# Kernel optimization log

Measured on AMD Instinct MI355X. Metric: run time of the kernel, lower is better.

Reference implementation:

```python
import jax, jax.numpy as jnp
import numpy as np

EPS = 1e-5

def layer_norm(x, g, b):
    m = jnp.mean(x, axis=-1, keepdims=True)
    v = jnp.var(x, axis=-1, keepdims=True)
    return (x - m) * jax.lax.rsqrt(v + EPS) * g + b

def setup_inputs() -> dict:
    key = jax.random.key(0)
    ks = jax.random.split(key, 16)
    B, N, C_Z, C_H = 1, 512, 128, 128
    s_z = 1.0 / np.sqrt(C_Z)
    s_h = 1.0 / np.sqrt(C_H)
    inp = {
        "z": jax.random.normal(ks[0], (B, N, N, C_Z), jnp.float32),
        "mask": jnp.ones((B, N, N), jnp.float32),
        # linear weights stored as [in, out] so forward is x @ W + b
        "w_ag": jax.random.uniform(ks[1], (C_Z, C_H), jnp.float32, -s_z, s_z),
        "b_ag": jnp.zeros((C_H,), jnp.float32),
        "w_ap": jax.random.uniform(ks[2], (C_Z, C_H), jnp.float32, -s_z, s_z),
        "b_ap": jnp.zeros((C_H,), jnp.float32),
        "w_bg": jax.random.uniform(ks[3], (C_Z, C_H), jnp.float32, -s_z, s_z),
        "b_bg": jnp.zeros((C_H,), jnp.float32),
        "w_bp": jax.random.uniform(ks[4], (C_Z, C_H), jnp.float32, -s_z, s_z),
        "b_bp": jnp.zeros((C_H,), jnp.float32),
        "w_g": jax.random.uniform(ks[5], (C_Z, C_Z), jnp.float32, -s_z, s_z),
        "b_g": jnp.zeros((C_Z,), jnp.float32),
        "w_z": jax.random.uniform(ks[6], (C_H, C_Z), jnp.float32, -s_h, s_h),
        "b_z": jnp.zeros((C_Z,), jnp.float32),
        "ln_in_g": jnp.ones((C_Z,), jnp.float32),
        "ln_in_b": jnp.zeros((C_Z,), jnp.float32),
        "ln_out_g": jnp.ones((C_H,), jnp.float32),
        "ln_out_b": jnp.zeros((C_H,), jnp.float32),
    }
    return inp

def reference(z, mask, w_ag, b_ag, w_ap, b_ap, w_bg, b_bg, w_bp, b_bp,
              w_g, b_g, w_z, b_z, ln_in_g, ln_in_b, ln_out_g, ln_out_b):
    m = mask[..., None]                      # [B,N,N,1]
    zn = layer_norm(z, ln_in_g, ln_in_b)     # [B,N,N,Cz]
    a = m * jax.nn.sigmoid(zn @ w_ag + b_ag) * (zn @ w_ap + b_ap)  # [B,N,N,Ch]
    b = m * jax.nn.sigmoid(zn @ w_bg + b_bg) * (zn @ w_bp + b_bp)  # [B,N,N,Ch]
    # outgoing: p[i,j,c] = sum_k a[i,k,c] * b[j,k,c]
    x = jnp.einsum('bikc,bjkc->bijc', a, b)
    x = layer_norm(x, ln_out_g, ln_out_b)
    x = x @ w_z + b_z
    g = jax.nn.sigmoid(zn @ w_g + b_g)
    return x * g
```

## Files before the change

kernel.cpp:

```cpp
#include <hip/hip_runtime.h>
#include <hip/hip_bf16.h>
#include <math.h>


#define N 512
#define C 128
#define NN (N*N)
#define PK 136
#define PT 40
#define PX 137

typedef __attribute__((ext_vector_type(8))) short bf16x8;
typedef __attribute__((ext_vector_type(4))) float f32x4;
typedef unsigned short u16;
typedef unsigned int u32;

__device__ __forceinline__ u16 f2bf(float f) {
    u32 u = __builtin_bit_cast(u32, f);
    u = (u + 0x7fffu + ((u >> 16) & 1u)) >> 16;
    return (u16)u;
}
__device__ __forceinline__ float bf2f(u16 h) {
    return __builtin_bit_cast(float, ((u32)h) << 16);
}
__device__ __forceinline__ float sigmoidf(float x) {
    return 1.f / (1.f + __expf(-x));
}

__global__ __launch_bounds__(256) void k_wt_all(
    const float* __restrict__ w0, const float* __restrict__ w1,
    const float* __restrict__ w2, const float* __restrict__ w3,
    const float* __restrict__ w4, const float* __restrict__ w5,
    u16* __restrict__ o0, u16* __restrict__ o1, u16* __restrict__ o2,
    u16* __restrict__ o3, u16* __restrict__ o4, u16* __restrict__ o5) {
    int sel = blockIdx.x >> 6;
    int idx = (blockIdx.x & 63) * 256 + threadIdx.x;
    const float* w = sel == 0 ? w0 : sel == 1 ? w1 : sel == 2 ? w2
                   : sel == 3 ? w3 : sel == 4 ? w4 : w5;
    u16* o = sel == 0 ? o0 : sel == 1 ? o1 : sel == 2 ? o2
           : sel == 3 ? o3 : sel == 4 ? o4 : o5;
    int co = idx >> 7, k = idx & 127;
    o[idx] = f2bf(w[k * C + co]);
}

__global__ __launch_bounds__(256) void k_proj_fused(
    const float* __restrict__ z, const float* __restrict__ mask,
    const float* __restrict__ lg, const float* __restrict__ lb,
    const u16* __restrict__ wag, const float* __restrict__ bag,
    const u16* __restrict__ wap, const float* __restrict__ bap,
    const u16* __restrict__ wbg, const float* __restrict__ bbg,
    const u16* __restrict__ wbp, const float* __restrict__ bbp,
    const u16* __restrict__ wgg, const float* __restrict__ bgg,
    u16* __restrict__ aT, u16* __restrict__ bT, u16* __restrict__ gate) {
    __shared__ u16 sA[64 * PK];
    __shared__ u16 sT[128 * 72];
    long r0 = (long)blockIdx.x * 64;
    int tid = threadIdx.x, wave = tid >> 6, lane = tid & 63;
    int lo = lane & 15, quad = lane >> 4;

    {
        int c = lane * 2;
        float g0 = lg[c], g1 = lg[c + 1], b0 = lb[c], b1 = lb[c + 1];
        for (int rr = 0; rr < 16; ++rr) {
            int row = wave * 16 + rr;
            float2 xv = *(const float2*)(z + (r0 + row) * C + c);
            float s = xv.x + xv.y, s2 = xv.x * xv.x + xv.y * xv.y;
#pragma unroll
            for (int off = 32; off; off >>= 1) {
                s += __shfl_xor(s, off);
                s2 += __shfl_xor(s2, off);
            }
            float mean = s * (1.f / 128.f);
            float var = s2 * (1.f / 128.f) - mean * mean;
            float rs = rsqrtf(var + 1e-5f);
            float y0 = (xv.x - mean) * rs * g0 + b0;
            float y1 = (xv.y - mean) * rs * g1 + b1;
            *(u32*)(&sA[row * PK + c]) = (u32)f2bf(y0) | ((u32)f2bf(y1) << 16);
        }
    }
    __syncthreads();

    int c0 = wave * 32;
    float msk[4][4];
#pragma unroll
    for (int mi = 0; mi < 4; ++mi)
#pragma unroll
        for (int r = 0; r < 4; ++r)
            msk[mi][r] = mask[r0 + mi * 16 + quad * 4 + r];

    auto pair_stage = [&](const u16* __restrict__ wG, const float* __restrict__ bG,
                          const u16* __restrict__ wP, const float* __restrict__ bP,
                          u16* __restrict__ outT) {
        bf16x8 fG[2][4], fP[2][4];
#pragma unroll
        for (int nt = 0; nt < 2; ++nt)
#pragma unroll
            for (int ki = 0; ki < 4; ++ki) {
                fG[nt][ki] = *(const bf16x8*)(wG + (c0 + nt * 16 + lo) * C + ki * 32 + quad * 8);
                fP[nt][ki] = *(const bf16x8*)(wP + (c0 + nt * 16 + lo) * C + ki * 32 + quad * 8);
            }
        f32x4 aG[4][2], aP[4][2];
#pragma unroll
        for (int mi = 0; mi < 4; ++mi)
#pragma unroll
            for (int nt = 0; nt < 2; ++nt) { aG[mi][nt] = (f32x4)(0.f); aP[mi][nt] = (f32x4)(0.f); }
#pragma unroll
        for (int mi = 0; mi < 4; ++mi)
#pragma unroll
            for (int ki = 0; ki < 4; ++ki) {
                bf16x8 av = *(const bf16x8*)(&sA[(mi * 16 + lo) * PK + ki * 32 + quad * 8]);
#pragma unroll
                for (int nt = 0; nt < 2; ++nt) {
                    aG[mi][nt] = __builtin_amdgcn_mfma_f32_16x16x32_bf16(av, fG[nt][ki], aG[mi][nt], 0, 0, 0);
                    aP[mi][nt] = __builtin_amdgcn_mfma_f32_16x16x32_bf16(av, fP[nt][ki], aP[mi][nt], 0, 0, 0);
                }
            }
#pragma unroll
        for (int nt = 0; nt < 2; ++nt) {
            int c = c0 + nt * 16 + lo;
            float bGv = bG[c], bPv = bP[c];
#pragma unroll
            for (int mi = 0; mi < 4; ++mi)
#pragma unroll
                for (int r = 0; r < 4; ++r) {
                    int row = mi * 16 + quad * 4 + r;
                    float val = msk[mi][r] * sigmoidf(aG[mi][nt][r] + bGv) * (aP[mi][nt][r] + bPv);
                    sT[c * 72 + row] = f2bf(val);
                }
        }
        __syncthreads();
#pragma unroll
        for (int p = 0; p < 4; ++p) {
            int linear = p * 2048 + tid * 8;
            int cc = linear >> 6, row = linear & 63;
            *(uint4*)(outT + (long)cc * NN + r0 + row) = *(const uint4*)(&sT[cc * 72 + row]);
        }
        __syncthreads();
    };
    pair_stage(wag, bag, wap, bap, aT);
    pair_stage(wbg, bbg, wbp, bbp, bT);

    {
        bf16x8 fG[2][4];
#pragma unroll
        for (int nt = 0; nt < 2; ++nt)
#pragma unroll
            for (int ki = 0; ki < 4; ++ki)
                fG[nt][ki] = *(const bf16x8*)(wgg + (c0 + nt * 16 + lo) * C + ki * 32 + quad * 8);
        f32x4 aG[4][2];
#pragma unroll
        for (int mi = 0; mi < 4; ++mi)
#pragma unroll
            for (int nt = 0; nt < 2; ++nt) aG[mi][nt] = (f32x4)(0.f);
#pragma unroll
        for (int mi = 0; mi < 4; ++mi)
#pragma unroll
            for (int ki = 0; ki < 4; ++ki) {
                bf16x8 av = *(const bf16x8*)(&sA[(mi * 16 + lo) * PK + ki * 32 + quad * 8]);
#pragma unroll
                for (int nt = 0; nt < 2; ++nt)
                    aG[mi][nt] = __builtin_amdgcn_mfma_f32_16x16x32_bf16(av, fG[nt][ki], aG[mi][nt], 0, 0, 0);
            }
        __syncthreads();
#pragma unroll
        for (int nt = 0; nt < 2; ++nt) {
            int c = c0 + nt * 16 + lo;
            float bv = bgg[c];
#pragma unroll
            for (int mi = 0; mi < 4; ++mi)
#pragma unroll
                for (int r = 0; r < 4; ++r) {
                    int row = mi * 16 + quad * 4 + r;
                    sA[row * PK + c] = f2bf(sigmoidf(aG[mi][nt][r] + bv));
                }
        }
        __syncthreads();
#pragma unroll
        for (int p = 0; p < 4; ++p) {
            int linear = p * 2048 + tid * 8;
            int row = linear >> 7, k = linear & 127;
            *(uint4*)(gate + (r0 + row) * C + k) = *(const uint4*)(&sA[row * PK + k]);
        }
    }
}

__global__ __launch_bounds__(256) void k_tri(const u16* __restrict__ aT,
                                             const u16* __restrict__ bT,
                                             u16* __restrict__ xT) {
    __shared__ u16 sA[128 * PT];
    __shared__ u16 sB[128 * PT];
    int c = blockIdx.y;
    int i0 = (blockIdx.x >> 2) * 128, j0 = (blockIdx.x & 3) * 128;
    const u16* aBase = aT + (long)c * NN + (long)i0 * N;
    const u16* bBase = bT + (long)c * NN + (long)j0 * N;
    int tid = threadIdx.x;
    int wave = tid >> 6, lane = tid & 63, lo = lane & 15, quad = lane >> 4;
    int mq = (wave >> 1) * 64, nq = (wave & 1) * 64;
    f32x4 acc[4][4];
#pragma unroll
    for (int mi = 0; mi < 4; ++mi)
#pragma unroll
        for (int ni = 0; ni < 4; ++ni) acc[mi][ni] = (f32x4)(0.f);
    for (int kk = 0; kk < N; kk += 32) {
        __syncthreads();
#pragma unroll
        for (int p = 0; p < 2; ++p) {
            int linear = p * 2048 + tid * 8;
            int row = linear >> 5, k = linear & 31;
            *(uint4*)(&sA[row * PT + k]) = *(const uint4*)(aBase + row * N + kk + k);
            *(uint4*)(&sB[row * PT + k]) = *(const uint4*)(bBase + row * N + kk + k);
        }
        __syncthreads();
        bf16x8 af[4], bfr[4];
#pragma unroll
        for (int mi = 0; mi < 4; ++mi)
            af[mi] = *(const bf16x8*)(&sA[(mq + mi * 16 + lo) * PT + quad * 8]);
#pragma unroll
        for (int ni = 0; ni < 4; ++ni)
            bfr[ni] = *(const bf16x8*)(&sB[(nq + ni * 16 + lo) * PT + quad * 8]);
#pragma unroll
        for (int mi = 0; mi < 4; ++mi)
#pragma unroll
            for (int ni = 0; ni < 4; ++ni)
                acc[mi][ni] = __builtin_amdgcn_mfma_f32_16x16x32_bf16(af[mi], bfr[ni], acc[mi][ni], 0, 0, 0);
    }
    u16* outBase = xT + (long)c * NN;
#pragma unroll
    for (int mi = 0; mi < 4; ++mi)
#pragma unroll
        for (int ni = 0; ni < 4; ++ni)
#pragma unroll
            for (int r = 0; r < 4; ++r) {
                int gi = i0 + mq + mi * 16 + quad * 4 + r;
                int gj = j0 + nq + ni * 16 + lo;
                outBase[(long)gi * N + gj] = f2bf(acc[mi][ni][r]);
            }
}

__global__ __launch_bounds__(256) void k_out(
    const u16* __restrict__ xT, const u16* __restrict__ gate,
    const u16* __restrict__ wzT, const float* __restrict__ bz,
    const float* __restrict__ lg, const float* __restrict__ lb,
    float* __restrict__ out) {
    __shared__ float sX[64 * PX];
    __shared__ u16 sA[64 * PK];
    __shared__ float sRed[2][4][64];
    __shared__ float2 sMV[64];
    long r0 = (long)blockIdx.x * 64;
    int tid = threadIdx.x;
#pragma unroll
    for (int p = 0; p < 4; ++p) {
        int linear = p * 2048 + tid * 8;
        int cc = linear >> 6, jr = linear & 63;
        uint4 v = *(const uint4*)(xT + (long)cc * NN + r0 + jr);
        u16* u = (u16*)&v;
#pragma unroll
        for (int e = 0; e < 8; ++e) sX[(jr + e) * PX + cc] = bf2f(u[e]);
    }
    __syncthreads();
    {
        int jr = tid & 63, part = tid >> 6;
        float s = 0, s2 = 0;
#pragma unroll
        for (int c = part * 32; c < part * 32 + 32; ++c) {
            float v = sX[jr * PX + c];
            s += v; s2 += v * v;
        }
        sRed[0][part][jr] = s; sRed[1][part][jr] = s2;
    }
    __syncthreads();
    if (tid < 64) {
        float S = 0, S2 = 0;
#pragma unroll
        for (int p = 0; p < 4; ++p) { S += sRed[0][p][tid]; S2 += sRed[1][p][tid]; }
        float mean = S * (1.f / 128.f);
        float var = S2 * (1.f / 128.f) - mean * mean;
        sMV[tid] = make_float2(mean, rsqrtf(var + 1e-5f));
    }
    __syncthreads();
    {
        int row = tid & 63, c0 = (tid >> 6) * 32;
        float2 mv = sMV[row];
#pragma unroll
        for (int c = c0; c < c0 + 32; ++c) {
            float v = (sX[row * PX + c] - mv.x) * mv.y * lg[c] + lb[c];
            sA[row * PK + c] = f2bf(v);
        }
    }
    __syncthreads();
    int wave = tid >> 6, lane = tid & 63, lo = lane & 15, quad = lane >> 4;
    int msub = wave * 16;
    bf16x8 av[4];
#pragma unroll
    for (int ki = 0; ki < 4; ++ki)
        av[ki] = *(const bf16x8*)(&sA[(msub + lo) * PK + ki * 32 + quad * 8]);
    f32x4 acc[8];
#pragma unroll
    for (int nt = 0; nt < 8; ++nt) acc[nt] = (f32x4)(0.f);
#pragma unroll
    for (int nt = 0; nt < 8; ++nt)
#pragma unroll
        for (int ki = 0; ki < 4; ++ki) {
            bf16x8 b8 = *(const bf16x8*)(wzT + (nt * 16 + lo) * C + ki * 32 + quad * 8);
            acc[nt] = __builtin_amdgcn_mfma_f32_16x16x32_bf16(av[ki], b8, acc[nt], 0, 0, 0);
        }
#pragma unroll
    for (int nt = 0; nt < 8; ++nt) {
        int c = nt * 16 + lo;
        float bzv = bz[c];
#pragma unroll
        for (int r = 0; r < 4; ++r) {
            int row = msub + quad * 4 + r;
            long rr = r0 + row;
            float g = bf2f(gate[rr * C + c]);
            out[rr * C + c] = (acc[nt][r] + bzv) * g;
        }
    }
}

extern "C" void kernel_launch(void* const* d_in, const int* in_sizes, int n_in,
                              void* d_out, int out_size, void* d_ws, size_t ws_size,
                              hipStream_t stream) {
    const float* z       = (const float*)d_in[0];
    const float* mask    = (const float*)d_in[1];
    const float* w_ag    = (const float*)d_in[2];
    const float* b_ag    = (const float*)d_in[3];
    const float* w_ap    = (const float*)d_in[4];
    const float* b_ap    = (const float*)d_in[5];
    const float* w_bg    = (const float*)d_in[6];
    const float* b_bg    = (const float*)d_in[7];
    const float* w_bp    = (const float*)d_in[8];
    const float* b_bp    = (const float*)d_in[9];
    const float* w_g     = (const float*)d_in[10];
    const float* b_g     = (const float*)d_in[11];
    const float* w_z     = (const float*)d_in[12];
    const float* b_z     = (const float*)d_in[13];
    const float* ln_in_g = (const float*)d_in[14];
    const float* ln_in_b = (const float*)d_in[15];
    const float* ln_out_g= (const float*)d_in[16];
    const float* ln_out_b= (const float*)d_in[17];
    float* out = (float*)d_out;

    char* ws = (char*)d_ws;
    u16* a_t  = (u16*)(ws);
    u16* b_t  = (u16*)(ws + 67108864L);
    u16* gate = (u16*)(ws + 134217728L);
    u16* x_t  = (u16*)(ws + 201326592L);
    u16* wag_t = (u16*)(ws + 268435456L);
    u16* wap_t = wag_t + 16384;
    u16* wbg_t = wag_t + 32768;
    u16* wbp_t = wag_t + 49152;
    u16* wg_t  = wag_t + 65536;
    u16* wz_t  = wag_t + 81920;

    k_wt_all<<<384, 256, 0, stream>>>(w_ag, w_ap, w_bg, w_bp, w_g, w_z,
                                      wag_t, wap_t, wbg_t, wbp_t, wg_t, wz_t);

    k_proj_fused<<<NN / 64, 256, 0, stream>>>(
        z, mask, ln_in_g, ln_in_b,
        wag_t, b_ag, wap_t, b_ap, wbg_t, b_bg, wbp_t, b_bp, wg_t, b_g,
        a_t, b_t, gate);

    k_tri<<<dim3(16, 128), 256, 0, stream>>>(a_t, b_t, x_t);

    k_out<<<NN / 64, 256, 0, stream>>>(x_t, gate, wz_t, b_z, ln_out_g, ln_out_b, out);
}
```

Measured before the change: 585.6 us.

## Fold layernorm affine into weights, per-wave transposes, prefetch and swizzle tri kernel

The layernorm gamma/beta are folded into the bf16 projection weights and into precomputed biases (a new k_bias kernel), so the projection and output kernels only normalize. The input layernorm now uses float4 loads with four lanes per row, and the projection kernel transposes through a small per-wave shared buffer instead of block-wide barriers. The triangle kernel gains register prefetch of the next k-tile and a swizzled 1D grid for better cache locality. These changes remove per-element affine work, reduce barriers, and hide global latency, at the cost of an extra small kernel launch and extra register pressure.

```diff
diff --git a/kernel.cpp b/kernel.cpp
--- a/kernel.cpp
+++ b/kernel.cpp
@@ -9,6 +9,7 @@
 #define PK 136
 #define PT 40
 #define PX 137
+#define ST 72
 
 typedef __attribute__((ext_vector_type(8))) short bf16x8;
 typedef __attribute__((ext_vector_type(4))) float f32x4;
@@ -31,6 +32,7 @@
     const float* __restrict__ w0, const float* __restrict__ w1,
     const float* __restrict__ w2, const float* __restrict__ w3,
     const float* __restrict__ w4, const float* __restrict__ w5,
+    const float* __restrict__ gin, const float* __restrict__ gout,
     u16* __restrict__ o0, u16* __restrict__ o1, u16* __restrict__ o2,
     u16* __restrict__ o3, u16* __restrict__ o4, u16* __restrict__ o5) {
     int sel = blockIdx.x >> 6;
@@ -39,43 +41,70 @@
                    : sel == 3 ? w3 : sel == 4 ? w4 : w5;
     u16* o = sel == 0 ? o0 : sel == 1 ? o1 : sel == 2 ? o2
            : sel == 3 ? o3 : sel == 4 ? o4 : o5;
+    const float* g = (sel == 5) ? gout : gin;
     int co = idx >> 7, k = idx & 127;
-    o[idx] = f2bf(w[k * C + co]);
+    o[idx] = f2bf(g[k] * w[k * C + co]);
+}
+
+__global__ __launch_bounds__(256) void k_bias(
+    const float* __restrict__ w0, const float* __restrict__ w1,
+    const float* __restrict__ w2, const float* __restrict__ w3,
+    const float* __restrict__ w4, const float* __restrict__ w5,
+    const float* __restrict__ b0, const float* __restrict__ b1,
+    const float* __restrict__ b2, const float* __restrict__ b3,
+    const float* __restrict__ b4, const float* __restrict__ b5,
+    const float* __restrict__ vin, const float* __restrict__ vout,
+    float* __restrict__ obias) {
+    int id = blockIdx.x * 256 + threadIdx.x;
+    int m = id >> 7, cc = id & 127;
+    const float* w = m == 0 ? w0 : m == 1 ? w1 : m == 2 ? w2
+                   : m == 3 ? w3 : m == 4 ? w4 : w5;
+    const float* b = m == 0 ? b0 : m == 1 ? b1 : m == 2 ? b2
+                   : m == 3 ? b3 : m == 4 ? b4 : b5;
+    const float* v = (m == 5) ? vout : vin;
+    float acc = 0.f;
+#pragma unroll 4
+    for (int k = 0; k < 128; ++k) acc += v[k] * w[k * C + cc];
+    obias[id] = b[cc] + acc;
 }
 
 __global__ __launch_bounds__(256) void k_proj_fused(
     const float* __restrict__ z, const float* __restrict__ mask,
-    const float* __restrict__ lg, const float* __restrict__ lb,
-    const u16* __restrict__ wag, const float* __restrict__ bag,
-    const u16* __restrict__ wap, const float* __restrict__ bap,
-    const u16* __restrict__ wbg, const float* __restrict__ bbg,
-    const u16* __restrict__ wbp, const float* __restrict__ bbp,
-    const u16* __restrict__ wgg, const float* __restrict__ bgg,
+    const u16* __restrict__ wag, const u16* __restrict__ wap,
+    const u16* __restrict__ wbg, const u16* __restrict__ wbp,
+    const u16* __restrict__ wgg, const float* __restrict__ biasAll,
     u16* __restrict__ aT, u16* __restrict__ bT, u16* __restrict__ gate) {
     __shared__ u16 sA[64 * PK];
-    __shared__ u16 sT[128 * 72];
+    __shared__ u16 sT[4][16 * ST];
     long r0 = (long)blockIdx.x * 64;
     int tid = threadIdx.x, wave = tid >> 6, lane = tid & 63;
     int lo = lane & 15, quad = lane >> 4;
 
     {
-        int c = lane * 2;
-        float g0 = lg[c], g1 = lg[c + 1], b0 = lb[c], b1 = lb[c + 1];
-        for (int rr = 0; rr < 16; ++rr) {
-            int row = wave * 16 + rr;
-            float2 xv = *(const float2*)(z + (r0 + row) * C + c);
-            float s = xv.x + xv.y, s2 = xv.x * xv.x + xv.y * xv.y;
-#pragma unroll
-            for (int off = 32; off; off >>= 1) {
-                s += __shfl_xor(s, off);
-                s2 += __shfl_xor(s2, off);
-            }
-            float mean = s * (1.f / 128.f);
-            float var = s2 * (1.f / 128.f) - mean * mean;
-            float rs = rsqrtf(var + 1e-5f);
-            float y0 = (xv.x - mean) * rs * g0 + b0;
-            float y1 = (xv.y - mean) * rs * g1 + b1;
-            *(u32*)(&sA[row * PK + c]) = (u32)f2bf(y0) | ((u32)f2bf(y1) << 16);
+        int rl = lane >> 2, cb = lane & 3;
+        int row = wave * 16 + rl;
+        const float* zr = z + (r0 + row) * C + cb * 32;
+        float4 v[8];
+        float s = 0.f, s2 = 0.f;
+#pragma unroll
+        for (int i = 0; i < 8; ++i) {
+            v[i] = *(const float4*)(zr + i * 4);
+            s  += v[i].x + v[i].y + v[i].z + v[i].w;
+            s2 += v[i].x * v[i].x + v[i].y * v[i].y + v[i].z * v[i].z + v[i].w * v[i].w;
+        }
+        s += __shfl_xor(s, 1); s2 += __shfl_xor(s2, 1);
+        s += __shfl_xor(s, 2); s2 += __shfl_xor(s2, 2);
+        float mean = s * (1.f / 128.f);
+        float rs = rsqrtf(s2 * (1.f / 128.f) - mean * mean + 1e-5f);
+        u16* dst = &sA[row * PK + cb * 32];
+#pragma unroll
+        for (int j = 0; j < 4; ++j) {
+            uint4 pk;
+            pk.x = (u32)f2bf((v[2*j].x   - mean) * rs) | ((u32)f2bf((v[2*j].y   - mean) * rs) << 16);
+            pk.y = (u32)f2bf((v[2*j].z   - mean) * rs) | ((u32)f2bf((v[2*j].w   - mean) * rs) << 16);
+            pk.z = (u32)f2bf((v[2*j+1].x - mean) * rs) | ((u32)f2bf((v[2*j+1].y - mean) * rs) << 16);
+            pk.w = (u32)f2bf((v[2*j+1].z - mean) * rs) | ((u32)f2bf((v[2*j+1].w - mean) * rs) << 16);
+            *(uint4*)(dst + 8 * j) = pk;
         }
     }
     __syncthreads();
@@ -87,92 +116,86 @@
 #pragma unroll
         for (int r = 0; r < 4; ++r)
             msk[mi][r] = mask[r0 + mi * 16 + quad * 4 + r];
+
+    u16* sTw = &sT[wave][0];
 
     auto pair_stage = [&](const u16* __restrict__ wG, const float* __restrict__ bG,
                           const u16* __restrict__ wP, const float* __restrict__ bP,
                           u16* __restrict__ outT) {
-        bf16x8 fG[2][4], fP[2][4];
-#pragma unroll
-        for (int nt = 0; nt < 2; ++nt)
-#pragma unroll
-            for (int ki = 0; ki < 4; ++ki) {
-                fG[nt][ki] = *(const bf16x8*)(wG + (c0 + nt * 16 + lo) * C + ki * 32 + quad * 8);
-                fP[nt][ki] = *(const bf16x8*)(wP + (c0 + nt * 16 + lo) * C + ki * 32 + quad * 8);
-            }
-        f32x4 aG[4][2], aP[4][2];
-#pragma unroll
-        for (int mi = 0; mi < 4; ++mi)
-#pragma unroll
-            for (int nt = 0; nt < 2; ++nt) { aG[mi][nt] = (f32x4)(0.f); aP[mi][nt] = (f32x4)(0.f); }
-#pragma unroll
-        for (int mi = 0; mi < 4; ++mi)
-#pragma unroll
-            for (int ki = 0; ki < 4; ++ki) {
-                bf16x8 av = *(const bf16x8*)(&sA[(mi * 16 + lo) * PK + ki * 32 + quad * 8]);
-#pragma unroll
-                for (int nt = 0; nt < 2; ++nt) {
-                    aG[mi][nt] = __builtin_amdgcn_mfma_f32_16x16x32_bf16(av, fG[nt][ki], aG[mi][nt], 0, 0, 0);
-                    aP[mi][nt] = __builtin_amdgcn_mfma_f32_16x16x32_bf16(av, fP[nt][ki], aP[mi][nt], 0, 0, 0);
-                }
-            }
 #pragma unroll
         for (int nt = 0; nt < 2; ++nt) {
             int c = c0 + nt * 16 + lo;
+            bf16x8 fG[4], fP[4];
+#pragma unroll
+            for (int ki = 0; ki < 4; ++ki) {
+                fG[ki] = *(const bf16x8*)(wG + c * C + ki * 32 + quad * 8);
+                fP[ki] = *(const bf16x8*)(wP + c * C + ki * 32 + quad * 8);
+            }
+            f32x4 aG[4], aP[4];
+#pragma unroll
+            for (int mi = 0; mi < 4; ++mi) { aG[mi] = (f32x4)(0.f); aP[mi] = (f32x4)(0.f); }
+#pragma unroll
+            for (int mi = 0; mi < 4; ++mi)
+#pragma unroll
+                for (int ki = 0; ki < 4; ++ki) {
+                    bf16x8 av = *(const bf16x8*)(&sA[(mi * 16 + lo) * PK + ki * 32 + quad * 8]);
+                    aG[mi] = __builtin_amdgcn_mfma_f32_16x16x32_bf16(av, fG[ki], aG[mi], 0, 0, 0);
+                    aP[mi] = __builtin_amdgcn_mfma_f32_16x16x32_bf16(av, fP[ki], aP[mi], 0, 0, 0);
+                }
             float bGv = bG[c], bPv = bP[c];
 #pragma unroll
+            for (int mi = 0; mi < 4; ++mi) {
+                float v0 = msk[mi][0] * sigmoidf(aG[mi][0] + bGv) * (aP[mi][0] + bPv);
+                float v1 = msk[mi][1] * sigmoidf(aG[mi][1] + bGv) * (aP[mi][1] + bPv);
+                float v2 = msk[mi][2] * sigmoidf(aG[mi][2] + bGv) * (aP[mi][2] + bPv);
+                float v3 = msk[mi][3] * sigmoidf(aG[mi][3] + bGv) * (aP[mi][3] + bPv);
+                uint2 pk;
+                pk.x = (u32)f2bf(v0) | ((u32)f2bf(v1) << 16);
+                pk.y = (u32)f2bf(v2) | ((u32)f2bf(v3) << 16);
+                *(uint2*)(&sTw[lo * ST + mi * 16 + quad * 4]) = pk;
+            }
+            {
+                int cl = lane >> 2, pr = lane & 3;
+                uint4 x0 = *(const uint4*)(&sTw[cl * ST + pr * 16]);
+                uint4 x1 = *(const uint4*)(&sTw[cl * ST + pr * 16 + 8]);
+                u16* g = outT + (long)(c0 + nt * 16 + cl) * NN + r0 + pr * 16;
+                *(uint4*)(g) = x0;
+                *(uint4*)(g + 8) = x1;
+            }
+        }
+    };
+    pair_stage(wag, biasAll + 0,   wap, biasAll + 128, aT);
+    pair_stage(wbg, biasAll + 256, wbp, biasAll + 384, bT);
+
+    {
+        f32x4 gA[2][4];
+#pragma unroll
+        for (int nt = 0; nt < 2; ++nt) {
+            bf16x8 gF[4];
+#pragma unroll
+            for (int ki = 0; ki < 4; ++ki)
+                gF[ki] = *(const bf16x8*)(wgg + (c0 + nt * 16 + lo) * C + ki * 32 + quad * 8);
+#pragma unroll
+            for (int mi = 0; mi < 4; ++mi) gA[nt][mi] = (f32x4)(0.f);
+#pragma unroll
             for (int mi = 0; mi < 4; ++mi)
 #pragma unroll
-                for (int r = 0; r < 4; ++r) {
-                    int row = mi * 16 + quad * 4 + r;
-                    float val = msk[mi][r] * sigmoidf(aG[mi][nt][r] + bGv) * (aP[mi][nt][r] + bPv);
-                    sT[c * 72 + row] = f2bf(val);
+                for (int ki = 0; ki < 4; ++ki) {
+                    bf16x8 av = *(const bf16x8*)(&sA[(mi * 16 + lo) * PK + ki * 32 + quad * 8]);
+                    gA[nt][mi] = __builtin_amdgcn_mfma_f32_16x16x32_bf16(av, gF[ki], gA[nt][mi], 0, 0, 0);
                 }
         }
         __syncthreads();
-#pragma unroll
-        for (int p = 0; p < 4; ++p) {
-            int linear = p * 2048 + tid * 8;
-            int cc = linear >> 6, row = linear & 63;
-            *(uint4*)(outT + (long)cc * NN + r0 + row) = *(const uint4*)(&sT[cc * 72 + row]);
-        }
-        __syncthreads();
-    };
-    pair_stage(wag, bag, wap, bap, aT);
-    pair_stage(wbg, bbg, wbp, bbp, bT);
-
-    {
-        bf16x8 fG[2][4];
-#pragma unroll
-        for (int nt = 0; nt < 2; ++nt)
-#pragma unroll
-            for (int ki = 0; ki < 4; ++ki)
-                fG[nt][ki] = *(const bf16x8*)(wgg + (c0 + nt * 16 + lo) * C + ki * 32 + quad * 8);
-        f32x4 aG[4][2];
-#pragma unroll
-        for (int mi = 0; mi < 4; ++mi)
-#pragma unroll
-            for (int nt = 0; nt < 2; ++nt) aG[mi][nt] = (f32x4)(0.f);
-#pragma unroll
-        for (int mi = 0; mi < 4; ++mi)
-#pragma unroll
-            for (int ki = 0; ki < 4; ++ki) {
-                bf16x8 av = *(const bf16x8*)(&sA[(mi * 16 + lo) * PK + ki * 32 + quad * 8]);
-#pragma unroll
-                for (int nt = 0; nt < 2; ++nt)
-                    aG[mi][nt] = __builtin_amdgcn_mfma_f32_16x16x32_bf16(av, fG[nt][ki], aG[mi][nt], 0, 0, 0);
-            }
-        __syncthreads();
+        const float* bg5 = biasAll + 512;
 #pragma unroll
         for (int nt = 0; nt < 2; ++nt) {
             int c = c0 + nt * 16 + lo;
-            float bv = bgg[c];
+            float bv = bg5[c];
 #pragma unroll
             for (int mi = 0; mi < 4; ++mi)
 #pragma unroll
-                for (int r = 0; r < 4; ++r) {
-                    int row = mi * 16 + quad * 4 + r;
-                    sA[row * PK + c] = f2bf(sigmoidf(aG[mi][nt][r] + bv));
-                }
+                for (int r = 0; r < 4; ++r)
+                    sA[(mi * 16 + quad * 4 + r) * PK + c] = f2bf(sigmoidf(gA[nt][mi][r] + bv));
         }
         __syncthreads();
 #pragma unroll
@@ -189,8 +212,10 @@
                                              u16* __restrict__ xT) {
     __shared__ u16 sA[128 * PT];
     __shared__ u16 sB[128 * PT];
-    int c = blockIdx.y;
-    int i0 = (blockIdx.x >> 2) * 128, j0 = (blockIdx.x & 3) * 128;
+    int bid = blockIdx.x;
+    int swz = (bid & 7) * 256 + (bid >> 3);
+    int c = swz >> 4;
+    int i0 = ((swz >> 2) & 3) * 128, j0 = (swz & 3) * 128;
     const u16* aBase = aT + (long)c * NN + (long)i0 * N;
     const u16* bBase = bT + (long)c * NN + (long)j0 * N;
     int tid = threadIdx.x;
@@ -201,16 +226,34 @@
     for (int mi = 0; mi < 4; ++mi)
 #pragma unroll
         for (int ni = 0; ni < 4; ++ni) acc[mi][ni] = (f32x4)(0.f);
+
+    int srow[2], sk[2];
+#pragma unroll
+    for (int p = 0; p < 2; ++p) {
+        int linear = p * 2048 + tid * 8;
+        srow[p] = linear >> 5; sk[p] = linear & 31;
+    }
+    uint4 ra[2], rb[2];
+#pragma unroll
+    for (int p = 0; p < 2; ++p) {
+        ra[p] = *(const uint4*)(aBase + srow[p] * N + sk[p]);
+        rb[p] = *(const uint4*)(bBase + srow[p] * N + sk[p]);
+    }
     for (int kk = 0; kk < N; kk += 32) {
         __syncthreads();
 #pragma unroll
         for (int p = 0; p < 2; ++p) {
-            int linear = p * 2048 + tid * 8;
-            int row = linear >> 5, k = linear & 31;
-            *(uint4*)(&sA[row * PT + k]) = *(const uint4*)(aBase + row * N + kk + k);
-            *(uint4*)(&sB[row * PT + k]) = *(const uint4*)(bBase + row * N + kk + k);
+            *(uint4*)(&sA[srow[p] * PT + sk[p]]) = ra[p];
+            *(uint4*)(&sB[srow[p] * PT + sk[p]]) = rb[p];
         }
         __syncthreads();
+        if (kk + 32 < N) {
+#pragma unroll
+            for (int p = 0; p < 2; ++p) {
+                ra[p] = *(const uint4*)(aBase + srow[p] * N + kk + 32 + sk[p]);
+                rb[p] = *(const uint4*)(bBase + srow[p] * N + kk + 32 + sk[p]);
+            }
+        }
         bf16x8 af[4], bfr[4];
 #pragma unroll
         for (int mi = 0; mi < 4; ++mi)
@@ -240,7 +283,6 @@
 __global__ __launch_bounds__(256) void k_out(
     const u16* __restrict__ xT, const u16* __restrict__ gate,
     const u16* __restrict__ wzT, const float* __restrict__ bz,
-    const float* __restrict__ lg, const float* __restrict__ lb,
     float* __restrict__ out) {
     __shared__ float sX[64 * PX];
     __shared__ u16 sA[64 * PK];
@@ -282,10 +324,8 @@
         int row = tid & 63, c0 = (tid >> 6) * 32;
         float2 mv = sMV[row];
 #pragma unroll
-        for (int c = c0; c < c0 + 32; ++c) {
-            float v = (sX[row * PX + c] - mv.x) * mv.y * lg[c] + lb[c];
-            sA[row * PK + c] = f2bf(v);
-        }
+        for (int c = c0; c < c0 + 32; ++c)
+            sA[row * PK + c] = f2bf((sX[row * PX + c] - mv.x) * mv.y);
     }
     __syncthreads();
     int wave = tid >> 6, lane = tid & 63, lo = lane & 15, quad = lane >> 4;
@@ -352,16 +392,21 @@
     u16* wbp_t = wag_t + 49152;
     u16* wg_t  = wag_t + 65536;
     u16* wz_t  = wag_t + 81920;
+    float* biasAdj = (float*)(ws + 268435456L + 196608L);
 
     k_wt_all<<<384, 256, 0, stream>>>(w_ag, w_ap, w_bg, w_bp, w_g, w_z,
+                                      ln_in_g, ln_out_g,
                                       wag_t, wap_t, wbg_t, wbp_t, wg_t, wz_t);
 
+    k_bias<<<3, 256, 0, stream>>>(w_ag, w_ap, w_bg, w_bp, w_g, w_z,
+                                  b_ag, b_ap, b_bg, b_bp, b_g, b_z,
+                                  ln_in_b, ln_out_b, biasAdj);
+
     k_proj_fused<<<NN / 64, 256, 0, stream>>>(
-        z, mask, ln_in_g, ln_in_b,
-        wag_t, b_ag, wap_t, b_ap, wbg_t, b_bg, wbp_t, b_bp, wg_t, b_g,
+        z, mask, wag_t, wap_t, wbg_t, wbp_t, wg_t, biasAdj,
         a_t, b_t, gate);
 
-    k_tri<<<dim3(16, 128), 256, 0, stream>>>(a_t, b_t, x_t);
-
-    k_out<<<NN / 64, 256, 0, stream>>>(x_t, gate, wz_t, b_z, ln_out_g, ln_out_b, out);
-}
+    k_tri<<<2048, 256, 0, stream>>>(a_t, b_t, x_t);
+
+    k_out<<<NN / 64, 256, 0, stream>>>(x_t, gate, wz_t, biasAdj + 640, out);
+}
```

Measured after the change: 669.8 us. 1.14x slower.
